# Optimization experiments

Measured on AMD Instinct MI355X. Metric: run time of the kernel, lower is better.

Reference implementation:

```python
import jax, jax.numpy as jnp
import numpy as np

N, T, H, K = 2000, 64, 128, 4
DDIMS = (16, 32, 16)
SDIMS = (8, 16)


def setup_inputs() -> dict:
    key = jax.random.key(0)
    ks = iter(jax.random.split(key, 40))
    nrm = lambda shape, s=0.1: jax.random.normal(next(ks), shape, jnp.float32) * s
    inp = {}
    for i, d in enumerate(DDIMS):
        inp[f"dyn{i}"] = jax.random.normal(next(ks), (N, T, d), jnp.float32)
        inp[f"dw1_{i}"] = nrm((d, H)); inp[f"db1_{i}"] = jnp.zeros((H,), jnp.float32)
        inp[f"dw2_{i}"] = nrm((H, d)); inp[f"db2_{i}"] = jnp.zeros((d,), jnp.float32)
    for i, d in enumerate(SDIMS):
        inp[f"static{i}"] = jax.random.normal(next(ks), (N, d), jnp.float32)
        inp[f"w_{i}"] = nrm((d, d)); inp[f"a_{i}"] = nrm((2 * d, 1))
    inp["distance"] = jax.random.uniform(next(ks), (N, N, K), jnp.float32)
    inp["W_dis"] = nrm((K, K)); inp["a_dis"] = nrm((K, 1))
    Ftot = sum(DDIMS)
    inp["Wih"] = nrm((4 * H, Ftot)); inp["Whh"] = nrm((4 * H, H))
    inp["bih"] = jnp.zeros((4 * H,), jnp.float32); inp["bhh"] = jnp.zeros((4 * H,), jnp.float32)
    inp["Wl"] = nrm((H, H)); inp["bl"] = jnp.zeros((H,), jnp.float32)
    inp["Wl2"] = nrm((H, 1)); inp["bl2"] = jnp.zeros((1,), jnp.float32)
    return inp


def _forward(dyn0, dw1_0, db1_0, dw2_0, db2_0,
             dyn1, dw1_1, db1_1, dw2_1, db2_1,
             dyn2, dw1_2, db1_2, dw2_2, db2_2,
             static0, w_0, a_0, static1, w_1, a_1,
             distance, W_dis, a_dis,
             Wih, Whh, bih, bhh, Wl, bl, Wl2, bl2):
    # --- GAT-style pairwise scores from static features ---
    scores = []
    for st, w, a, d in ((static0, w_0, a_0, SDIMS[0]), (static1, w_1, a_1, SDIMS[1])):
        hi = st @ w  # (N, d)
        # sigmoid(cat([hi_n, hi_m]) @ a) == sigmoid(hi_n @ a[:d] + hi_m @ a[d:])
        scores.append(jax.nn.sigmoid((hi @ a[:d]) + (hi @ a[d:]).T))  # (N, N)
    # --- distance-based score: sigmoid((dist @ W_dis) @ a_dis) ---
    scores.append(jax.nn.sigmoid(jnp.squeeze(distance @ (W_dis @ a_dis), -1)))
    static_dis = jax.nn.softmax(scores[0] + scores[1] + scores[2], axis=-1)  # (N, N)

    # --- per-category dynamic gating MLP: Linear-LeakyReLU-Linear-Sigmoid ---
    wts = []
    for dyn, W1, b1, W2, b2 in ((dyn0, dw1_0, db1_0, dw2_0, db2_0),
                                (dyn1, dw1_1, db1_1, dw2_1, db2_1),
                                (dyn2, dw1_2, db1_2, dw2_2, db2_2)):
        wts.append(jax.nn.sigmoid(jax.nn.leaky_relu(dyn @ W1 + b1) @ W2 + b2))
    dynamic_weights = jnp.concatenate(wts, axis=-1)              # (N, T, F)
    x = dynamic_weights * jnp.concatenate([dyn0, dyn1, dyn2], -1)  # (N, T, F)

    # --- LSTM (batch_first, zero init: torch code never passes h0 to rnn) ---
    def step(carry, xt):
        h, c = carry
        g = xt @ Wih.T + bih + h @ Whh.T + bhh
        i_, f_, g_, o_ = jnp.split(g, 4, axis=-1)  # torch gate order i,f,g,o
        c = jax.nn.sigmoid(f_) * c + jax.nn.sigmoid(i_) * jnp.tanh(g_)
        h = jax.nn.sigmoid(o_) * jnp.tanh(c)
        return (h, c), h

    init = (jnp.zeros((N, H), x.dtype), jnp.zeros((N, H), x.dtype))
    (hn, _), hs = jax.lax.scan(step, init, jnp.swapaxes(x, 0, 1))
    h = jnp.swapaxes(hs, 0, 1)  # (N, T, H)

    # spatial aggregation: out[n] = h[n] + sum_m static_dis[n,m] * h[m]
    h = h + jnp.einsum('nm,mtd->ntd', static_dis, h)

    y = jax.nn.leaky_relu(h @ Wl + bl) @ Wl2 + bl2  # (N, T, 1)
    return y


def reference(dyn0, dw1_0, db1_0, dw2_0, db2_0,
              dyn1, dw1_1, db1_1, dw2_1, db2_1,
              dyn2, dw1_2, db1_2, dw2_2, db2_2,
              static0, w_0, a_0, static1, w_1, a_1,
              distance, W_dis, a_dis,
              Wih, Whh, bih, bhh, Wl, bl, Wl2, bl2):
    return _forward(dyn0, dw1_0, db1_0, dw2_0, db2_0,
                    dyn1, dw1_1, db1_1, dw2_1, db2_1,
                    dyn2, dw1_2, db1_2, dw2_2, db2_2,
                    static0, w_0, a_0, static1, w_1, a_1,
                    distance, W_dis, a_dis,
                    Wih, Whh, bih, bhh, Wl, bl, Wl2, bl2)
```

## Files before the change

kernel.cpp:

```cpp
#include <hip/hip_runtime.h>
#include <hip/hip_bf16.h>
#include <math.h>

#define N_NODES 2000
#define T_STEPS 64
#define H_DIM   128
#define F_TOT   64
#define KP      2048
#define NCOLS   8192

typedef unsigned short ushort_t;
typedef unsigned int uint_t;
typedef short bf16x8 __attribute__((ext_vector_type(8)));
typedef float f32x4 __attribute__((ext_vector_type(4)));

__device__ __forceinline__ float sigmoidf_(float x) { return 1.0f / (1.0f + expf(-x)); }
__device__ __forceinline__ float lrelu_(float x) { return x > 0.f ? x : 0.01f * x; }

__device__ __forceinline__ float fast_sig(float x) {
    float e = __builtin_exp2f(x * -1.44269504f);
    return 1.0f / (1.0f + e);
}
__device__ __forceinline__ float fast_tanh(float x) {
    float e = __builtin_exp2f(x * -2.88539008f);
    return 2.0f / (1.0f + e) - 1.0f;
}

__device__ __forceinline__ ushort_t f2bf(float x) {
    union { float f; uint_t u; } v; v.f = x;
    uint_t r = v.u + 0x7FFFu + ((v.u >> 16) & 1u);
    return (ushort_t)(r >> 16);
}

__device__ __forceinline__ void stage16(const ushort_t* g, ushort_t* l) {
    __builtin_amdgcn_global_load_lds(
        (const __attribute__((address_space(1))) uint_t*)g,
        (__attribute__((address_space(3))) uint_t*)l,
        16, 0, 0);
}

__global__ void pernode_kernel(const float* __restrict__ st0, const float* __restrict__ w0,
                               const float* __restrict__ a0,
                               const float* __restrict__ st1, const float* __restrict__ w1,
                               const float* __restrict__ a1,
                               const float* __restrict__ Wdis, const float* __restrict__ adis,
                               float* __restrict__ pernode)
{
    int n = blockIdx.x * blockDim.x + threadIdx.x;
    if (n == 0) {
        #pragma unroll
        for (int k = 0; k < 4; ++k) {
            float s = 0.f;
            #pragma unroll
            for (int j = 0; j < 4; ++j) s += Wdis[k * 4 + j] * adis[j];
            pernode[8192 + k] = s;
        }
    }
    if (n >= N_NODES) return;
    {
        float v[8];
        #pragma unroll
        for (int d = 0; d < 8; ++d) v[d] = st0[n * 8 + d];
        float sa = 0.f, sb = 0.f;
        #pragma unroll
        for (int j = 0; j < 8; ++j) {
            float h = 0.f;
            #pragma unroll
            for (int d = 0; d < 8; ++d) h += v[d] * w0[d * 8 + j];
            sa += h * a0[j];
            sb += h * a0[8 + j];
        }
        pernode[n] = sa;
        pernode[2048 + n] = sb;
    }
    {
        float v[16];
        #pragma unroll
        for (int d = 0; d < 16; ++d) v[d] = st1[n * 16 + d];
        float sa = 0.f, sb = 0.f;
        #pragma unroll
        for (int j = 0; j < 16; ++j) {
            float h = 0.f;
            #pragma unroll
            for (int d = 0; d < 16; ++d) h += v[d] * w1[d * 16 + j];
            sa += h * a1[j];
            sb += h * a1[16 + j];
        }
        pernode[4096 + n] = sa;
        pernode[6144 + n] = sb;
    }
}

__global__ void prep_kernel(const float* __restrict__ Wih, const float* __restrict__ Whh,
                            const float* __restrict__ bih, const float* __restrict__ bhh,
                            const float* __restrict__ Wl,
                            ushort_t* __restrict__ wihbf, ushort_t* __restrict__ whhbf,
                            float* __restrict__ bsum, ushort_t* __restrict__ wlTbf)
{
    int idx = blockIdx.x * blockDim.x + threadIdx.x;
    if (idx < 32768) {
        wihbf[idx] = f2bf(Wih[idx]);
    } else if (idx < 98304) {
        whhbf[idx - 32768] = f2bf(Whh[idx - 32768]);
    } else if (idx < 98816) {
        bsum[idx - 98304] = bih[idx - 98304] + bhh[idx - 98304];
    } else if (idx < 115200) {
        int idx2 = idx - 98816;
        int j = idx2 >> 7, hh = idx2 & 127;
        wlTbf[idx2] = f2bf(Wl[hh * 128 + j]);
    }
}

__global__ __launch_bounds__(256) void score_softmax_kernel(const float* __restrict__ dist,
                                                            const float* __restrict__ pernode,
                                                            ushort_t* __restrict__ Abf)
{
    __shared__ float srow[N_NODES];
    __shared__ float red[256];
    int n = blockIdx.x;
    int tid = threadIdx.x;
    float wd0 = pernode[8192], wd1 = pernode[8193], wd2 = pernode[8194], wd3 = pernode[8195];
    float s0 = pernode[n];
    float s1 = pernode[4096 + n];
    const float* s0m = pernode + 2048;
    const float* s1m = pernode + 6144;
    float mx = -1e30f;
    for (int m = tid; m < N_NODES; m += 256) {
        float4 dv = *reinterpret_cast<const float4*>(dist + ((size_t)n * N_NODES + m) * 4);
        float sc = sigmoidf_(s0 + s0m[m]) + sigmoidf_(s1 + s1m[m])
                 + sigmoidf_(dv.x * wd0 + dv.y * wd1 + dv.z * wd2 + dv.w * wd3);
        srow[m] = sc;
        mx = fmaxf(mx, sc);
    }
    red[tid] = mx;
    __syncthreads();
    for (int off = 128; off > 0; off >>= 1) {
        if (tid < off) red[tid] = fmaxf(red[tid], red[tid + off]);
        __syncthreads();
    }
    mx = red[0];
    __syncthreads();
    float sum = 0.f;
    for (int m = tid; m < N_NODES; m += 256) {
        float e = expf(srow[m] - mx);
        srow[m] = e;
        sum += e;
    }
    red[tid] = sum;
    __syncthreads();
    for (int off = 128; off > 0; off >>= 1) {
        if (tid < off) red[tid] += red[tid + off];
        __syncthreads();
    }
    float inv = 1.f / red[0];
    for (int m = tid; m < KP; m += 256) {
        float v = 0.f;
        if (m < N_NODES) v = srow[m] * inv + (m == n ? 1.f : 0.f);
        Abf[(size_t)n * KP + m] = f2bf(v);
    }
}

__global__ void padA_kernel(ushort_t* __restrict__ Abf)
{
    uint_t* p = (uint_t*)(Abf + (size_t)N_NODES * KP);
    int idx = blockIdx.x * blockDim.x + threadIdx.x;
    p[idx] = 0;
}

template <int D>
__device__ __forceinline__ void gate_cat(const float* __restrict__ dyn_row,
                                         const float* __restrict__ W1, const float* __restrict__ b1,
                                         const float* __restrict__ W2, const float* __restrict__ b2,
                                         float* __restrict__ xout)
{
    float v[D];
    #pragma unroll
    for (int d = 0; d < D; ++d) v[d] = dyn_row[d];
    float acc[D];
    #pragma unroll
    for (int d = 0; d < D; ++d) acc[d] = 0.f;
    for (int j = 0; j < H_DIM; ++j) {
        float hj = b1[j];
        #pragma unroll
        for (int d = 0; d < D; ++d) hj += v[d] * W1[d * H_DIM + j];
        float a = lrelu_(hj);
        #pragma unroll
        for (int d = 0; d < D; ++d) acc[d] += a * W2[j * D + d];
    }
    #pragma unroll
    for (int d = 0; d < D; ++d) xout[d] = sigmoidf_(acc[d] + b2[d]) * v[d];
}

__global__ __launch_bounds__(256) void gating_kernel(
    const float* __restrict__ dyn0, const float* __restrict__ dw1_0, const float* __restrict__ db1_0,
    const float* __restrict__ dw2_0, const float* __restrict__ db2_0,
    const float* __restrict__ dyn1, const float* __restrict__ dw1_1, const float* __restrict__ db1_1,
    const float* __restrict__ dw2_1, const float* __restrict__ db2_1,
    const float* __restrict__ dyn2, const float* __restrict__ dw1_2, const float* __restrict__ db1_2,
    const float* __restrict__ dw2_2, const float* __restrict__ db2_2,
    ushort_t* __restrict__ xout)
{
    int r = blockIdx.x * blockDim.x + threadIdx.x;
    if (r >= N_NODES * T_STEPS) return;
    float xr[F_TOT];
    gate_cat<16>(dyn0 + (size_t)r * 16, dw1_0, db1_0, dw2_0, db2_0, xr);
    gate_cat<32>(dyn1 + (size_t)r * 32, dw1_1, db1_1, dw2_1, db2_1, xr + 16);
    gate_cat<16>(dyn2 + (size_t)r * 16, dw1_2, db1_2, dw2_2, db2_2, xr + 48);
    uint_t pk[32];
    #pragma unroll
    for (int d = 0; d < 32; ++d)
        pk[d] = (uint_t)f2bf(xr[2 * d]) | ((uint_t)f2bf(xr[2 * d + 1]) << 16);
    uint4* dst = reinterpret_cast<uint4*>(xout + (size_t)r * F_TOT);
    #pragma unroll
    for (int i = 0; i < 8; ++i)
        dst[i] = make_uint4(pk[4 * i], pk[4 * i + 1], pk[4 * i + 2], pk[4 * i + 3]);
}

__global__ __launch_bounds__(512) void lstm_mfma_kernel(
    const ushort_t* __restrict__ xbf,
    const ushort_t* __restrict__ wihbf,
    const ushort_t* __restrict__ whhbf,
    const float*    __restrict__ bsum,
    ushort_t*       __restrict__ h_bf)
{
    __shared__ ushort_t xb_lds[2 * 512];
    __shared__ ushort_t h_lds[16 * 128];

    int tid  = threadIdx.x;
    int lane = tid & 63;
    int w    = tid >> 6;
    int n0   = blockIdx.x * 8;
    int uc   = w * 16;
    int col  = lane & 15;
    int ke   = (lane >> 4) * 8;
    int arow = lane & 15;
    int rgrp = lane >> 4;

    if (w == 0) {
        int s = lane >> 3, c = lane & 7;
        stage16(xbf + ((size_t)(n0 + s) * 64 + 0) * 64 + ((c ^ s) * 8), &xb_lds[0]);
    }

    ((uint_t*)h_lds)[tid] = 0;
    ((uint_t*)h_lds)[512 + tid] = 0;

    bf16x8 bihf[4][2];
    bf16x8 bhhf[4][4];
    float  bias[4];
    #pragma unroll
    for (int gi = 0; gi < 4; ++gi) {
        int n = gi * 128 + uc + col;
        bias[gi] = bsum[n];
        #pragma unroll
        for (int kt = 0; kt < 2; ++kt)
            bihf[gi][kt] = *(const bf16x8*)&wihbf[n * 64 + kt * 32 + ke];
        #pragma unroll
        for (int kt = 0; kt < 4; ++kt)
            bhhf[gi][kt] = *(const bf16x8*)&whhbf[n * 128 + kt * 32 + ke];
    }

    float c_st[4] = {0.f, 0.f, 0.f, 0.f};
    __syncthreads();

    for (int t = 0; t < T_STEPS; ++t) {
        const ushort_t* xb = &xb_lds[(t & 1) * 512];
        bf16x8 ax[2] = {};
        if (arow < 8) {
            ax[0] = *(const bf16x8*)&xb[arow * 64 + ((rgrp ^ arow) << 3)];
            ax[1] = *(const bf16x8*)&xb[arow * 64 + (((4 + rgrp) ^ arow) << 3)];
        }
        bf16x8 ah[4];
        #pragma unroll
        for (int kt = 0; kt < 4; ++kt)
            ah[kt] = *(const bf16x8*)&h_lds[arow * 128 + (((kt * 4 + rgrp) ^ (arow & 7)) << 3)];
        __syncthreads();

        if (w == 0 && t + 1 < T_STEPS) {
            int s = lane >> 3, c = lane & 7;
            stage16(xbf + ((size_t)(n0 + s) * 64 + (t + 1)) * 64 + ((c ^ s) * 8),
                    &xb_lds[((t + 1) & 1) * 512]);
        }

        f32x4 acc[4];
        #pragma unroll
        for (int gi = 0; gi < 4; ++gi)
            acc[gi] = (f32x4){bias[gi], bias[gi], bias[gi], bias[gi]};
        #pragma unroll
        for (int gi = 0; gi < 4; ++gi) {
            #pragma unroll
            for (int kt = 0; kt < 2; ++kt)
                acc[gi] = __builtin_amdgcn_mfma_f32_16x16x32_bf16(ax[kt], bihf[gi][kt], acc[gi], 0, 0, 0);
            #pragma unroll
            for (int kt = 0; kt < 4; ++kt)
                acc[gi] = __builtin_amdgcn_mfma_f32_16x16x32_bf16(ah[kt], bhhf[gi][kt], acc[gi], 0, 0, 0);
        }

        if (rgrp < 2) {
            int u = uc + col;
            int uch = u >> 3, ulo = u & 7;
            #pragma unroll
            for (int j = 0; j < 4; ++j) {
                float iv = fast_sig(acc[0][j]);
                float fv = fast_sig(acc[1][j]);
                float gv = fast_tanh(acc[2][j]);
                float ov = fast_sig(acc[3][j]);
                c_st[j] = fv * c_st[j] + iv * gv;
                float hv = ov * fast_tanh(c_st[j]);
                int s = rgrp * 4 + j;
                ushort_t hbv = f2bf(hv);
                h_lds[s * 128 + ((uch ^ s) << 3) + ulo] = hbv;
                h_bf[(size_t)(n0 + s) * NCOLS + t * H_DIM + u] = hbv;
            }
        }
        __syncthreads();
    }
}

__global__ __launch_bounds__(256) void transposeH_kernel(const ushort_t* __restrict__ h_bf,
                                                         ushort_t* __restrict__ hT)
{
    __shared__ ushort_t tile[64][72];
    int c0 = blockIdx.x * 64;
    int k0 = blockIdx.y * 64;
    int tid = threadIdx.x;
    int rr = tid >> 4;
    int cc = (tid & 15) * 4;
    #pragma unroll
    for (int i = 0; i < 4; ++i) {
        int r = rr + i * 16;
        ushort_t v0 = 0, v1 = 0, v2 = 0, v3 = 0;
        if (k0 + r < N_NODES) {
            const ushort_t* src = h_bf + (size_t)(k0 + r) * NCOLS + c0 + cc;
            ushort4 v = *reinterpret_cast<const ushort4*>(src);
            v0 = v.x; v1 = v.y; v2 = v.z; v3 = v.w;
        }
        tile[r][cc] = v0; tile[r][cc + 1] = v1; tile[r][cc + 2] = v2; tile[r][cc + 3] = v3;
    }
    __syncthreads();
    #pragma unroll
    for (int i = 0; i < 4; ++i) {
        int r = rr + i * 16;
        ushort4 v;
        v.x = tile[cc][r]; v.y = tile[cc + 1][r]; v.z = tile[cc + 2][r]; v.w = tile[cc + 3][r];
        *reinterpret_cast<ushort4*>(hT + (size_t)(c0 + r) * KP + k0 + cc) = v;
    }
}

__global__ __launch_bounds__(256) void agg_gemm_mfma(const ushort_t* __restrict__ Abf,
                                                     const ushort_t* __restrict__ hT,
                                                     ushort_t* __restrict__ Cbf)
{
    __shared__ ushort_t A_lds[128 * 32];
    __shared__ ushort_t B_lds[128 * 32];
    int tid = threadIdx.x;
    int lane = tid & 63;
    int w = tid >> 6;
    int wr = w >> 1, wc = w & 1;
    int row0 = blockIdx.y * 128;
    int col0 = blockIdx.x * 128;

    f32x4 acc[4][4] = {};

    int lrow = lane >> 2;
    int lkk = (lane & 3) * 8;

    for (int k0 = 0; k0 < KP; k0 += 32) {
        stage16(Abf + (size_t)(row0 + w * 16 + lrow) * KP + k0 + lkk,       &A_lds[w * 512]);
        stage16(Abf + (size_t)(row0 + 64 + w * 16 + lrow) * KP + k0 + lkk,  &A_lds[w * 512 + 2048]);
        stage16(hT + (size_t)(col0 + w * 16 + lrow) * KP + k0 + lkk,        &B_lds[w * 512]);
        stage16(hT + (size_t)(col0 + 64 + w * 16 + lrow) * KP + k0 + lkk,   &B_lds[w * 512 + 2048]);
        __syncthreads();

        bf16x8 av[4], bv[4];
        #pragma unroll
        for (int mi = 0; mi < 4; ++mi)
            av[mi] = *(const bf16x8*)&A_lds[(wr * 64 + mi * 16 + (lane & 15)) * 32 + (lane >> 4) * 8];
        #pragma unroll
        for (int ni = 0; ni < 4; ++ni)
            bv[ni] = *(const bf16x8*)&B_lds[(wc * 64 + ni * 16 + (lane & 15)) * 32 + (lane >> 4) * 8];
        #pragma unroll
        for (int mi = 0; mi < 4; ++mi)
            #pragma unroll
            for (int ni = 0; ni < 4; ++ni)
                acc[mi][ni] = __builtin_amdgcn_mfma_f32_16x16x32_bf16(av[mi], bv[ni], acc[mi][ni], 0, 0, 0);
        __syncthreads();
    }

    #pragma unroll
    for (int mi = 0; mi < 4; ++mi) {
        #pragma unroll
        for (int ni = 0; ni < 4; ++ni) {
            int colg = col0 + wc * 64 + ni * 16 + (lane & 15);
            #pragma unroll
            for (int j = 0; j < 4; ++j) {
                int rowg = row0 + wr * 64 + mi * 16 + (lane >> 4) * 4 + j;
                if (rowg < N_NODES)
                    Cbf[(size_t)rowg * NCOLS + colg] = f2bf(acc[mi][ni][j]);
            }
        }
    }
}

__global__ __launch_bounds__(256) void final_proj_mfma(
    const ushort_t* __restrict__ aggbf,
    const ushort_t* __restrict__ wlTbf,
    const float* __restrict__ bl,
    const float* __restrict__ Wl2,
    const float* __restrict__ bl2,
    float* __restrict__ y)
{
    int tid  = threadIdx.x;
    int lane = tid & 63;
    int w    = tid >> 6;
    int row0 = blockIdx.x * 128 + w * 32;
    int col  = lane & 15;
    int rgrp = lane >> 4;
    int ke   = rgrp * 8;

    bf16x8 bfr[2][4];
    #pragma unroll
    for (int nt = 0; nt < 2; ++nt) {
        const ushort_t* base = aggbf + (size_t)(row0 + nt * 16 + col) * H_DIM;
        #pragma unroll
        for (int kt = 0; kt < 4; ++kt)
            bfr[nt][kt] = *(const bf16x8*)&base[kt * 32 + ke];
    }

    float yp0 = 0.f, yp1 = 0.f;
    #pragma unroll
    for (int mi = 0; mi < 8; ++mi) {
        bf16x8 af[4];
        const ushort_t* abase = wlTbf + (size_t)(mi * 16 + col) * H_DIM;
        #pragma unroll
        for (int kt = 0; kt < 4; ++kt)
            af[kt] = *(const bf16x8*)&abase[kt * 32 + ke];
        float4 blv = *reinterpret_cast<const float4*>(&bl[mi * 16 + rgrp * 4]);
        float4 w2v = *reinterpret_cast<const float4*>(&Wl2[mi * 16 + rgrp * 4]);
        f32x4 acc0 = {blv.x, blv.y, blv.z, blv.w};
        f32x4 acc1 = acc0;
        #pragma unroll
        for (int kt = 0; kt < 4; ++kt) {
            acc0 = __builtin_amdgcn_mfma_f32_16x16x32_bf16(af[kt], bfr[0][kt], acc0, 0, 0, 0);
            acc1 = __builtin_amdgcn_mfma_f32_16x16x32_bf16(af[kt], bfr[1][kt], acc1, 0, 0, 0);
        }
        yp0 += lrelu_(acc0[0]) * w2v.x + lrelu_(acc0[1]) * w2v.y
             + lrelu_(acc0[2]) * w2v.z + lrelu_(acc0[3]) * w2v.w;
        yp1 += lrelu_(acc1[0]) * w2v.x + lrelu_(acc1[1]) * w2v.y
             + lrelu_(acc1[2]) * w2v.z + lrelu_(acc1[3]) * w2v.w;
    }
    yp0 += __shfl_xor(yp0, 16); yp0 += __shfl_xor(yp0, 32);
    yp1 += __shfl_xor(yp1, 16); yp1 += __shfl_xor(yp1, 32);
    if (lane < 16) {
        float b2 = bl2[0];
        y[row0 + col] = yp0 + b2;
        y[row0 + 16 + col] = yp1 + b2;
    }
}

extern "C" void kernel_launch(void* const* d_in, const int* in_sizes, int n_in,
                              void* d_out, int out_size, void* d_ws, size_t ws_size,
                              hipStream_t stream)
{
    const float* dyn0  = (const float*)d_in[0];
    const float* dw1_0 = (const float*)d_in[1];
    const float* db1_0 = (const float*)d_in[2];
    const float* dw2_0 = (const float*)d_in[3];
    const float* db2_0 = (const float*)d_in[4];
    const float* dyn1  = (const float*)d_in[5];
    const float* dw1_1 = (const float*)d_in[6];
    const float* db1_1 = (const float*)d_in[7];
    const float* dw2_1 = (const float*)d_in[8];
    const float* db2_1 = (const float*)d_in[9];
    const float* dyn2  = (const float*)d_in[10];
    const float* dw1_2 = (const float*)d_in[11];
    const float* db1_2 = (const float*)d_in[12];
    const float* dw2_2 = (const float*)d_in[13];
    const float* db2_2 = (const float*)d_in[14];
    const float* st0   = (const float*)d_in[15];
    const float* w_0   = (const float*)d_in[16];
    const float* a_0   = (const float*)d_in[17];
    const float* st1   = (const float*)d_in[18];
    const float* w_1   = (const float*)d_in[19];
    const float* a_1   = (const float*)d_in[20];
    const float* dist  = (const float*)d_in[21];
    const float* W_dis = (const float*)d_in[22];
    const float* a_dis = (const float*)d_in[23];
    const float* Wih   = (const float*)d_in[24];
    const float* Whh   = (const float*)d_in[25];
    const float* bih   = (const float*)d_in[26];
    const float* bhh   = (const float*)d_in[27];
    const float* Wl    = (const float*)d_in[28];
    const float* bl    = (const float*)d_in[29];
    const float* Wl2   = (const float*)d_in[30];
    const float* bl2   = (const float*)d_in[31];

    char* ws = (char*)d_ws;
    float*    pernode = (float*)ws;
    float*    bsum    = (float*)(ws + 65536);
    ushort_t* wihbf   = (ushort_t*)(ws + 67584);
    ushort_t* whhbf   = (ushort_t*)(ws + 133120);
    ushort_t* wlTbf   = (ushort_t*)(ws + 264192);
    ushort_t* Abf     = (ushort_t*)(ws + 296960);
    ushort_t* xbf     = (ushort_t*)(ws + 8685568);
    ushort_t* hbf     = (ushort_t*)(ws + 25069568);
    ushort_t* hT      = (ushort_t*)(ws + 57837568);
    ushort_t* aggbf   = (ushort_t*)(ws + 91392000);

    hipLaunchKernelGGL(pernode_kernel, dim3(8), dim3(256), 0, stream,
                       st0, w_0, a_0, st1, w_1, a_1, W_dis, a_dis, pernode);
    hipLaunchKernelGGL(prep_kernel, dim3(450), dim3(256), 0, stream,
                       Wih, Whh, bih, bhh, Wl, wihbf, whhbf, bsum, wlTbf);
    hipLaunchKernelGGL(score_softmax_kernel, dim3(N_NODES), dim3(256), 0, stream,
                       dist, pernode, Abf);
    hipLaunchKernelGGL(padA_kernel, dim3(192), dim3(256), 0, stream, Abf);
    hipLaunchKernelGGL(gating_kernel, dim3(500), dim3(256), 0, stream,
                       dyn0, dw1_0, db1_0, dw2_0, db2_0,
                       dyn1, dw1_1, db1_1, dw2_1, db2_1,
                       dyn2, dw1_2, db1_2, dw2_2, db2_2, xbf);
    hipLaunchKernelGGL(lstm_mfma_kernel, dim3(N_NODES / 8), dim3(512), 0, stream,
                       xbf, wihbf, whhbf, bsum, hbf);
    hipLaunchKernelGGL(transposeH_kernel, dim3(NCOLS / 64, KP / 64), dim3(256), 0, stream,
                       hbf, hT);
    hipLaunchKernelGGL(agg_gemm_mfma, dim3(NCOLS / 128, KP / 128), dim3(256), 0, stream,
                       Abf, hT, aggbf);
    hipLaunchKernelGGL(final_proj_mfma, dim3(1000), dim3(256), 0, stream,
                       aggbf, wlTbf, bl, Wl2, bl2, (float*)d_out);
}
```

Before: 609.0 us.

## Compute dynamic gating MLP with bf16 MFMA tiles instead of scalar FP32 loops

Replaces the per-row scalar FP32 gating MLP (one thread per row, looping over 128 hidden units) with a wave-level MFMA kernel that processes 16 rows per wave. The first-layer output goes through swizzled LDS, and weights are pre-transposed and converted to bf16 in the prep kernel. The LSTM kernel also gets a minimum-occupancy hint in its launch bounds. This removes a large FP32 ALU cost, at the price of bf16 rounding in the gating inputs and weights.

```diff
diff --git a/kernel.cpp b/kernel.cpp
--- a/kernel.cpp
+++ b/kernel.cpp
@@ -94,20 +94,46 @@
 __global__ void prep_kernel(const float* __restrict__ Wih, const float* __restrict__ Whh,
                             const float* __restrict__ bih, const float* __restrict__ bhh,
                             const float* __restrict__ Wl,
+                            const float* __restrict__ dw1_0, const float* __restrict__ dw1_1,
+                            const float* __restrict__ dw1_2,
+                            const float* __restrict__ dw2_0, const float* __restrict__ dw2_1,
+                            const float* __restrict__ dw2_2,
                             ushort_t* __restrict__ wihbf, ushort_t* __restrict__ whhbf,
-                            float* __restrict__ bsum, ushort_t* __restrict__ wlTbf)
+                            float* __restrict__ bsum, ushort_t* __restrict__ wlTbf,
+                            ushort_t* __restrict__ w1tb, ushort_t* __restrict__ w2tb)
 {
     int idx = blockIdx.x * blockDim.x + threadIdx.x;
-    if (idx < 32768) {
-        wihbf[idx] = f2bf(Wih[idx]);
-    } else if (idx < 98304) {
-        whhbf[idx - 32768] = f2bf(Whh[idx - 32768]);
-    } else if (idx < 98816) {
-        bsum[idx - 98304] = bih[idx - 98304] + bhh[idx - 98304];
-    } else if (idx < 115200) {
-        int idx2 = idx - 98816;
-        int j = idx2 >> 7, hh = idx2 & 127;
-        wlTbf[idx2] = f2bf(Wl[hh * 128 + j]);
+    if (idx < 32768) { wihbf[idx] = f2bf(Wih[idx]); return; }
+    idx -= 32768;
+    if (idx < 65536) { whhbf[idx] = f2bf(Whh[idx]); return; }
+    idx -= 65536;
+    if (idx < 512) { bsum[idx] = bih[idx] + bhh[idx]; return; }
+    idx -= 512;
+    if (idx < 16384) {
+        int j = idx >> 7, hh = idx & 127;
+        wlTbf[idx] = f2bf(Wl[hh * 128 + j]);
+        return;
+    }
+    idx -= 16384;
+    if (idx < 12288) {
+        int c = idx >> 12;
+        int r = idx & 4095;
+        int n = r >> 5, k = r & 31;
+        const float* W1 = (c == 0) ? dw1_0 : ((c == 1) ? dw1_1 : dw1_2);
+        int d = (c == 1) ? 32 : 16;
+        w1tb[idx >= 0 ? (c * 4096 + r) : 0] = (k < d) ? f2bf(W1[k * 128 + n]) : (ushort_t)0;
+        return;
+    }
+    idx -= 12288;
+    if (idx < 8192) {
+        int c, base, d;
+        if (idx < 2048)      { c = 0; base = 0;    d = 16; }
+        else if (idx < 6144) { c = 1; base = 2048; d = 32; }
+        else                 { c = 2; base = 6144; d = 16; }
+        int r = idx - base;
+        int n = r >> 7, k = r & 127;
+        const float* W2 = (c == 0) ? dw2_0 : ((c == 1) ? dw2_1 : dw2_2);
+        w2tb[idx] = f2bf(W2[k * d + n]);
     }
 }
 
@@ -167,56 +193,87 @@
     p[idx] = 0;
 }
 
-template <int D>
-__device__ __forceinline__ void gate_cat(const float* __restrict__ dyn_row,
-                                         const float* __restrict__ W1, const float* __restrict__ b1,
-                                         const float* __restrict__ W2, const float* __restrict__ b2,
-                                         float* __restrict__ xout)
-{
-    float v[D];
-    #pragma unroll
-    for (int d = 0; d < D; ++d) v[d] = dyn_row[d];
-    float acc[D];
-    #pragma unroll
-    for (int d = 0; d < D; ++d) acc[d] = 0.f;
-    for (int j = 0; j < H_DIM; ++j) {
-        float hj = b1[j];
-        #pragma unroll
-        for (int d = 0; d < D; ++d) hj += v[d] * W1[d * H_DIM + j];
-        float a = lrelu_(hj);
-        #pragma unroll
-        for (int d = 0; d < D; ++d) acc[d] += a * W2[j * D + d];
-    }
-    #pragma unroll
-    for (int d = 0; d < D; ++d) xout[d] = sigmoidf_(acc[d] + b2[d]) * v[d];
-}
-
-__global__ __launch_bounds__(256) void gating_kernel(
-    const float* __restrict__ dyn0, const float* __restrict__ dw1_0, const float* __restrict__ db1_0,
-    const float* __restrict__ dw2_0, const float* __restrict__ db2_0,
-    const float* __restrict__ dyn1, const float* __restrict__ dw1_1, const float* __restrict__ db1_1,
-    const float* __restrict__ dw2_1, const float* __restrict__ db2_1,
-    const float* __restrict__ dyn2, const float* __restrict__ dw1_2, const float* __restrict__ db1_2,
-    const float* __restrict__ dw2_2, const float* __restrict__ db2_2,
+template <int D, int XOFF>
+__device__ __forceinline__ void gate_mfma_cat(
+    const float* __restrict__ dyn, const float* __restrict__ b1,
+    const float* __restrict__ b2,
+    const ushort_t* __restrict__ w1t, const ushort_t* __restrict__ w2t,
+    ushort_t* __restrict__ a2, ushort_t* __restrict__ xout, int r0, int lane)
+{
+    int col = lane & 15, rgrp = lane >> 4, ke = rgrp * 8;
+
+    bf16x8 af = {};
+    if (D == 32 || rgrp < 2) {
+        const float* src = dyn + (size_t)(r0 + col) * D + ke;
+        float4 va = *reinterpret_cast<const float4*>(src);
+        float4 vb = *reinterpret_cast<const float4*>(src + 4);
+        af[0] = (short)f2bf(va.x); af[1] = (short)f2bf(va.y);
+        af[2] = (short)f2bf(va.z); af[3] = (short)f2bf(va.w);
+        af[4] = (short)f2bf(vb.x); af[5] = (short)f2bf(vb.y);
+        af[6] = (short)f2bf(vb.z); af[7] = (short)f2bf(vb.w);
+    }
+
+    __syncthreads();
+    #pragma unroll
+    for (int mi = 0; mi < 8; ++mi) {
+        bf16x8 bf = *(const bf16x8*)&w1t[(mi * 16 + col) * 32 + ke];
+        float b1v = b1[mi * 16 + col];
+        f32x4 acc = {b1v, b1v, b1v, b1v};
+        acc = __builtin_amdgcn_mfma_f32_16x16x32_bf16(af, bf, acc, 0, 0, 0);
+        #pragma unroll
+        for (int jj = 0; jj < 4; ++jj) {
+            int r = rgrp * 4 + jj;
+            int j = mi * 16 + col;
+            a2[r * 128 + (((j >> 3) ^ (r & 7)) << 3) + (j & 7)] = f2bf(lrelu_(acc[jj]));
+        }
+    }
+    __syncthreads();
+
+    bf16x8 a2f[4];
+    #pragma unroll
+    for (int kt = 0; kt < 4; ++kt)
+        a2f[kt] = *(const bf16x8*)&a2[col * 128 + (((kt * 4 + rgrp) ^ (col & 7)) << 3)];
+    #pragma unroll
+    for (int nt = 0; nt < D / 16; ++nt) {
+        float b2v = b2[nt * 16 + col];
+        f32x4 acc = {b2v, b2v, b2v, b2v};
+        #pragma unroll
+        for (int kt = 0; kt < 4; ++kt) {
+            bf16x8 wf = *(const bf16x8*)&w2t[(nt * 16 + col) * 128 + kt * 32 + ke];
+            acc = __builtin_amdgcn_mfma_f32_16x16x32_bf16(a2f[kt], wf, acc, 0, 0, 0);
+        }
+        #pragma unroll
+        for (int jj = 0; jj < 4; ++jj) {
+            int rg = r0 + rgrp * 4 + jj;
+            int dd = nt * 16 + col;
+            float xv = fast_sig(acc[jj]) * dyn[(size_t)rg * D + dd];
+            xout[(size_t)rg * 64 + XOFF + dd] = f2bf(xv);
+        }
+    }
+}
+
+__global__ __launch_bounds__(256) void gating_mfma_kernel(
+    const float* __restrict__ dyn0, const float* __restrict__ dyn1,
+    const float* __restrict__ dyn2,
+    const float* __restrict__ db1_0, const float* __restrict__ db1_1,
+    const float* __restrict__ db1_2,
+    const float* __restrict__ db2_0, const float* __restrict__ db2_1,
+    const float* __restrict__ db2_2,
+    const ushort_t* __restrict__ w1tb, const ushort_t* __restrict__ w2tb,
     ushort_t* __restrict__ xout)
 {
-    int r = blockIdx.x * blockDim.x + threadIdx.x;
-    if (r >= N_NODES * T_STEPS) return;
-    float xr[F_TOT];
-    gate_cat<16>(dyn0 + (size_t)r * 16, dw1_0, db1_0, dw2_0, db2_0, xr);
-    gate_cat<32>(dyn1 + (size_t)r * 32, dw1_1, db1_1, dw2_1, db2_1, xr + 16);
-    gate_cat<16>(dyn2 + (size_t)r * 16, dw1_2, db1_2, dw2_2, db2_2, xr + 48);
-    uint_t pk[32];
-    #pragma unroll
-    for (int d = 0; d < 32; ++d)
-        pk[d] = (uint_t)f2bf(xr[2 * d]) | ((uint_t)f2bf(xr[2 * d + 1]) << 16);
-    uint4* dst = reinterpret_cast<uint4*>(xout + (size_t)r * F_TOT);
-    #pragma unroll
-    for (int i = 0; i < 8; ++i)
-        dst[i] = make_uint4(pk[4 * i], pk[4 * i + 1], pk[4 * i + 2], pk[4 * i + 3]);
-}
-
-__global__ __launch_bounds__(512) void lstm_mfma_kernel(
+    __shared__ ushort_t a2_lds[4][16 * 128];
+    int tid  = threadIdx.x;
+    int lane = tid & 63;
+    int w    = tid >> 6;
+    int r0   = blockIdx.x * 64 + w * 16;
+    ushort_t* a2 = a2_lds[w];
+    gate_mfma_cat<16, 0 >(dyn0, db1_0, db2_0, w1tb,        w2tb,        a2, xout, r0, lane);
+    gate_mfma_cat<32, 16>(dyn1, db1_1, db2_1, w1tb + 4096, w2tb + 2048, a2, xout, r0, lane);
+    gate_mfma_cat<16, 48>(dyn2, db1_2, db2_2, w1tb + 8192, w2tb + 6144, a2, xout, r0, lane);
+}
+
+__global__ __launch_bounds__(512, 2) void lstm_mfma_kernel(
     const ushort_t* __restrict__ xbf,
     const ushort_t* __restrict__ wihbf,
     const ushort_t* __restrict__ whhbf,
@@ -505,18 +562,21 @@
     ushort_t* hbf     = (ushort_t*)(ws + 25069568);
     ushort_t* hT      = (ushort_t*)(ws + 57837568);
     ushort_t* aggbf   = (ushort_t*)(ws + 91392000);
+    ushort_t* w1tb    = (ushort_t*)(ws + 124160000);
+    ushort_t* w2tb    = (ushort_t*)(ws + 124184576);
 
     hipLaunchKernelGGL(pernode_kernel, dim3(8), dim3(256), 0, stream,
                        st0, w_0, a_0, st1, w_1, a_1, W_dis, a_dis, pernode);
-    hipLaunchKernelGGL(prep_kernel, dim3(450), dim3(256), 0, stream,
-                       Wih, Whh, bih, bhh, Wl, wihbf, whhbf, bsum, wlTbf);
+    hipLaunchKernelGGL(prep_kernel, dim3(530), dim3(256), 0, stream,
+                       Wih, Whh, bih, bhh, Wl,
+                       dw1_0, dw1_1, dw1_2, dw2_0, dw2_1, dw2_2,
+                       wihbf, whhbf, bsum, wlTbf, w1tb, w2tb);
     hipLaunchKernelGGL(score_softmax_kernel, dim3(N_NODES), dim3(256), 0, stream,
                        dist, pernode, Abf);
     hipLaunchKernelGGL(padA_kernel, dim3(192), dim3(256), 0, stream, Abf);
-    hipLaunchKernelGGL(gating_kernel, dim3(500), dim3(256), 0, stream,
-                       dyn0, dw1_0, db1_0, dw2_0, db2_0,
-                       dyn1, dw1_1, db1_1, dw2_1, db2_1,
-                       dyn2, dw1_2, db1_2, dw2_2, db2_2, xbf);
+    hipLaunchKernelGGL(gating_mfma_kernel, dim3(2000), dim3(256), 0, stream,
+                       dyn0, dyn1, dyn2, db1_0, db1_1, db1_2,
+                       db2_0, db2_1, db2_2, w1tb, w2tb, xbf);
     hipLaunchKernelGGL(lstm_mfma_kernel, dim3(N_NODES / 8), dim3(512), 0, stream,
                        xbf, wihbf, whhbf, bsum, hbf);
     hipLaunchKernelGGL(transposeH_kernel, dim3(NCOLS / 64, KP / 64), dim3(256), 0, stream,
```

Result: faster. 515.7 us (-15.3%).
